# Optimization experiments

Measured on AMD Instinct MI355X. Metric: run time of the kernel, lower is better.

Reference implementation:

```python
import jax, jax.numpy as jnp
import numpy as np

T, B, I, H = 100, 64, 256, 512


def setup_inputs() -> dict:
    key = jax.random.key(0)
    ks = jax.random.split(key, 7)
    # torch kaiming_uniform_(a=sqrt(5)) + fan_in bias init -> uniform(-1/sqrt(fan_in), 1/sqrt(fan_in))
    b_ih = 1.0 / np.sqrt(I)
    b_hh = 1.0 / np.sqrt(H)
    return {
        "input": jax.random.normal(ks[0], (T, B, I), jnp.float32),
        "initial_h": jax.random.normal(ks[1], (B, H), jnp.float32),
        "initial_c": jax.random.normal(ks[2], (B, H), jnp.float32),
        "weight_ih": jax.random.uniform(ks[3], (4 * H, I), jnp.float32, -b_ih, b_ih),
        "weight_hh": jax.random.uniform(ks[4], (4 * H, H), jnp.float32, -b_hh, b_hh),
        "bias_ih": jax.random.uniform(ks[5], (4 * H,), jnp.float32, -b_ih, b_ih),
        "bias_hh": jax.random.uniform(ks[6], (4 * H,), jnp.float32, -b_hh, b_hh),
    }


def reference(input, initial_h, initial_c, weight_ih, weight_hh, bias_ih, bias_hh):
    Bsz, Isz = input.shape[1], input.shape[2]
    Hs = initial_h.shape[1]

    def step(carry, x_t):
        hx, cx, ev_ih, ev_hh, ev_b = carry
        # standard LSTM gates, torch gate order: i, f, g, o
        gates = x_t @ weight_ih.T + hx @ weight_hh.T + bias_ih + bias_hh  # [B,4H]
        i_g, f_g, g_g, o_g = jnp.split(gates, 4, axis=1)
        i = jax.nn.sigmoid(i_g)
        f = jax.nn.sigmoid(f_g)
        g = jnp.tanh(g_g)
        o = jax.nn.sigmoid(o_g)
        cy = f * cx + i * g
        hy = o * jnp.tanh(cy)
        # e-prop instantaneous derivatives of c_t wrt the i/f/g pre-activations
        d_i = g * i * (1.0 - i)          # [B,H]
        d_f = cx * f * (1.0 - f)
        d_g = i * (1.0 - g * g)
        d = jnp.concatenate([d_i, d_f, d_g], axis=1)[:, :, None]  # [B,3H,1]
        f3 = jnp.tile(f, (1, 3))[:, :, None]                      # [B,3H,1]
        # eligibility-trace recursion: ev_t = f_t * ev_{t-1} + d_t (outer) input
        ev_ih = f3 * ev_ih + d * x_t[:, None, :]   # [B,3H,I]
        ev_hh = f3 * ev_hh + d * hx[:, None, :]    # [B,3H,H]
        ev_b = f3 * ev_b + d                       # [B,3H,1]
        return (hy, cy, ev_ih, ev_hh, ev_b), hy

    ev_ih0 = jnp.zeros((Bsz, 3 * Hs, Isz), input.dtype)
    ev_hh0 = jnp.zeros((Bsz, 3 * Hs, Hs), input.dtype)
    ev_b0 = jnp.zeros((Bsz, 3 * Hs, 1), input.dtype)
    (hx, cx, ev_ih, ev_hh, ev_b), outputs = jax.lax.scan(
        step, (initial_h, initial_c, ev_ih0, ev_hh0, ev_b0), input
    )
    return outputs, cx, ev_ih, ev_hh, ev_b
```

## Files before the change

kernel.cpp:

```cpp
#include <hip/hip_runtime.h>
#include <math.h>

#define TT 100
#define BB 64
#define II 256
#define HH 512
#define G4H 2048
#define G3H 1536

#define OFF_GT    0
#define OFF_HBUF  13107200
#define OFF_FBUF  16416768
#define OFF_DBUF  19693568
#define OFF_CT    29523968
#define OFF_XT    29556736
#define OFF_WIHT  31195136
#define OFF_WHHT  31719424

#define O_OUT   0
#define O_CX    3276800
#define O_EVIH  3309568
#define O_EVHH  28475392
#define O_EVB   78807040

__global__ __launch_bounds__(256) void tp64(const float* __restrict__ src,
                                            float* __restrict__ dst,
                                            int R, int C,
                                            long sstride, long dstride) {
  __shared__ float tile[64][65];
  src += (long)blockIdx.z * sstride;
  dst += (long)blockIdx.z * dstride;
  int r0 = blockIdx.y * 64, c0 = blockIdx.x * 64;
  int tx = threadIdx.x & 15, tq = threadIdx.x >> 4;
#pragma unroll
  for (int p = 0; p < 4; ++p) {
    int rl = p * 16 + tq;
    float4 v = *(const float4*)(src + (long)(r0 + rl) * C + c0 + tx * 4);
    tile[rl][tx * 4 + 0] = v.x; tile[rl][tx * 4 + 1] = v.y;
    tile[rl][tx * 4 + 2] = v.z; tile[rl][tx * 4 + 3] = v.w;
  }
  __syncthreads();
#pragma unroll
  for (int p = 0; p < 4; ++p) {
    int cl = p * 16 + tq;
    float4 v;
    v.x = tile[tx * 4 + 0][cl]; v.y = tile[tx * 4 + 1][cl];
    v.z = tile[tx * 4 + 2][cl]; v.w = tile[tx * 4 + 3][cl];
    *(float4*)(dst + (long)(c0 + cl) * R + r0 + tx * 4) = v;
  }
}

__global__ __launch_bounds__(256) void make_whhg(const float* __restrict__ WhhT,
                                                 float* __restrict__ WhhG) {
  int gid = blockIdx.x * 256 + threadIdx.x;
  int k = gid >> 11, j = gid & 2047;
  float v = WhhT[gid];
  WhhG[(long)k * G4H + ((j & 511) << 2) + (j >> 9)] = v;
}

template <int BK, int KTILES, bool BIAS, bool ZSHIFT>
__global__ __launch_bounds__(256) void gemm_tn(
    const float* __restrict__ A, long batchA, int lda,
    const float* __restrict__ Z, long batchZ, int ldz,
    const float* __restrict__ Z0, long batchZ0,
    float* __restrict__ C, long batchC, int ldc,
    const float* __restrict__ bia, const float* __restrict__ bib) {
  __shared__ float As[BK][64];
  __shared__ float Zs[BK][64];
  int tid = threadIdx.x;
  int tn = tid & 15, tm = tid >> 4;
  int m0 = blockIdx.x * 64, n0 = blockIdx.y * 64;
  long bz = blockIdx.z;
  const float* Ab = A + bz * batchA + m0;
  const float* Zb = Z + bz * batchZ + n0;
  const float* Z0b = ZSHIFT ? (Z0 + bz * batchZ0 + n0) : nullptr;
  float acc[4][4] = {};
  for (int kt = 0; kt < KTILES; ++kt) {
    int k0 = kt * BK;
#pragma unroll
    for (int p = tid; p < BK * 64; p += 256) {
      int r = p >> 6, c = p & 63;
      int k = k0 + r;
      As[r][c] = Ab[(long)k * lda + c];
      const float* zr;
      if (ZSHIFT)
        zr = (k == 0) ? Z0b : (Zb + (long)(k - 1) * ldz);
      else
        zr = Zb + (long)k * ldz;
      Zs[r][c] = zr[c];
    }
    __syncthreads();
#pragma unroll 4
    for (int kk = 0; kk < BK; ++kk) {
      float4 a = *(const float4*)&As[kk][tm * 4];
      float4 z = *(const float4*)&Zs[kk][tn * 4];
      float av[4] = {a.x, a.y, a.z, a.w};
      float zv[4] = {z.x, z.y, z.z, z.w};
#pragma unroll
      for (int q = 0; q < 4; ++q)
#pragma unroll
        for (int r = 0; r < 4; ++r)
          acc[q][r] = fmaf(av[q], zv[r], acc[q][r]);
    }
    __syncthreads();
  }
  float* Cb = C + bz * batchC + n0 + tn * 4;
#pragma unroll
  for (int q = 0; q < 4; ++q) {
    int m = m0 + tm * 4 + q;
    float bv = BIAS ? (bia[m] + bib[m]) : 0.f;
    float4 v;
    v.x = acc[q][0] + bv; v.y = acc[q][1] + bv;
    v.z = acc[q][2] + bv; v.w = acc[q][3] + bv;
    *(float4*)(Cb + (long)m * ldc) = v;
  }
}

__global__ __launch_bounds__(512) void lstm_step2(const float* __restrict__ G_T,
                                                  const float* __restrict__ WhhG,
                                                  float* __restrict__ Hbuf,
                                                  float* __restrict__ cT,
                                                  float* __restrict__ Fbuf,
                                                  float* __restrict__ Dbuf,
                                                  int t) {
  __shared__ float red[2][4][4][64];
  int tid = threadIdx.x;
  int lane = tid & 63;
  int wave = __builtin_amdgcn_readfirstlane(tid >> 6);
  int hl = wave & 1, kp = wave >> 1;
  int hh = blockIdx.x * 2 + hl;
  float a0 = 0.f, a1 = 0.f, a2 = 0.f, a3 = 0.f;
  const float* hp = Hbuf + (long)t * (HH * BB) + kp * 128 * BB + lane;
  const float* wp = WhhG + (long)(kp * 128) * G4H + hh * 4;
#pragma unroll 4
  for (int k = 0; k < 128; ++k) {
    float h = hp[(long)k * BB];
    float4 w = *(const float4*)(wp + (long)k * G4H);
    a0 = fmaf(w.x, h, a0);
    a1 = fmaf(w.y, h, a1);
    a2 = fmaf(w.z, h, a2);
    a3 = fmaf(w.w, h, a3);
  }
  red[hl][kp][0][lane] = a0;
  red[hl][kp][1][lane] = a1;
  red[hl][kp][2][lane] = a2;
  red[hl][kp][3][lane] = a3;
  __syncthreads();
  if (tid < 128) {
    int b = tid & 63, h2 = tid >> 6;
    int hhx = blockIdx.x * 2 + h2;
    const float* gp = G_T + (long)t * (G4H * BB) + hhx * BB + b;
    float g[4];
#pragma unroll
    for (int q = 0; q < 4; ++q)
      g[q] = gp[(long)q * (HH * BB)] + red[h2][0][q][b] + red[h2][1][q][b] +
             red[h2][2][q][b] + red[h2][3][q][b];
    float ig = 1.f / (1.f + expf(-g[0]));
    float fg = 1.f / (1.f + expf(-g[1]));
    float gg = tanhf(g[2]);
    float og = 1.f / (1.f + expf(-g[3]));
    int idx = hhx * BB + b;
    float co = cT[idx];
    float cy = fg * co + ig * gg;
    cT[idx] = cy;
    Hbuf[(long)(t + 1) * (HH * BB) + idx] = og * tanhf(cy);
    Fbuf[(long)t * (HH * BB) + idx] = fg;
    float* dp = Dbuf + (long)t * (G3H * BB) + idx;
    dp[0] = gg * ig * (1.f - ig);
    dp[HH * BB] = co * fg * (1.f - fg);
    dp[2 * HH * BB] = ig * (1.f - gg * gg);
  }
}

__global__ __launch_bounds__(256) void suffix_scale(float* __restrict__ Dbuf,
                                                    const float* __restrict__ Fbuf,
                                                    float* __restrict__ evb) {
  int g = blockIdx.x * 256 + threadIdx.x;
  int b = g & 63, hh = g >> 6;
  float P = 1.f, e0 = 0.f, e1 = 0.f, e2 = 0.f;
#pragma unroll 2
  for (int t = TT - 1; t >= 0; --t) {
    float* dp = Dbuf + (long)t * (G3H * BB) + hh * BB + b;
    float v0 = dp[0] * P, v1 = dp[HH * BB] * P, v2 = dp[2 * HH * BB] * P;
    dp[0] = v0; dp[HH * BB] = v1; dp[2 * HH * BB] = v2;
    e0 += v0; e1 += v1; e2 += v2;
    P *= Fbuf[(long)t * (HH * BB) + hh * BB + b];
  }
  evb[b * G3H + hh] = e0;
  evb[b * G3H + HH + hh] = e1;
  evb[b * G3H + 2 * HH + hh] = e2;
}

extern "C" void kernel_launch(void* const* d_in, const int* in_sizes, int n_in,
                              void* d_out, int out_size, void* d_ws, size_t ws_size,
                              hipStream_t stream) {
  const float* x   = (const float*)d_in[0];
  const float* h0  = (const float*)d_in[1];
  const float* c0  = (const float*)d_in[2];
  const float* Wih = (const float*)d_in[3];
  const float* Whh = (const float*)d_in[4];
  const float* bih = (const float*)d_in[5];
  const float* bhh = (const float*)d_in[6];
  float* out = (float*)d_out;
  float* ws = (float*)d_ws;

  float* G_T   = ws + OFF_GT;
  float* DbufT = ws + OFF_GT;
  float* Hbuf  = ws + OFF_HBUF;
  float* Fbuf  = ws + OFF_FBUF;
  float* Dbuf  = ws + OFF_DBUF;
  float* cT    = ws + OFF_CT;
  float* xT    = ws + OFF_XT;
  float* WhhG  = ws + OFF_XT;
  float* WihT  = ws + OFF_WIHT;
  float* WhhT  = ws + OFF_WHHT;

  tp64<<<dim3(II / 64, G4H / 64, 1), 256, 0, stream>>>(Wih, WihT, G4H, II, 0, 0);
  tp64<<<dim3(HH / 64, G4H / 64, 1), 256, 0, stream>>>(Whh, WhhT, G4H, HH, 0, 0);
  tp64<<<dim3(II / 64, 1, TT), 256, 0, stream>>>(x, xT, BB, II, BB * II, BB * II);
  tp64<<<dim3(HH / 64, 1, 1), 256, 0, stream>>>(h0, Hbuf, BB, HH, 0, 0);
  tp64<<<dim3(HH / 64, 1, 1), 256, 0, stream>>>(c0, cT, BB, HH, 0, 0);

  gemm_tn<64, 4, true, false><<<dim3(G4H / 64, 1, TT), 256, 0, stream>>>(
      WihT, 0, G4H, xT, (long)II * BB, BB, nullptr, 0,
      G_T, (long)G4H * BB, BB, bih, bhh);

  make_whhg<<<dim3(HH * G4H / 256, 1, 1), 256, 0, stream>>>(WhhT, WhhG);

  for (int t = 0; t < TT; ++t) {
    lstm_step2<<<dim3(HH / 2, 1, 1), 512, 0, stream>>>(G_T, WhhG, Hbuf, cT,
                                                       Fbuf, Dbuf, t);
  }

  suffix_scale<<<dim3(HH * BB / 256, 1, 1), 256, 0, stream>>>(Dbuf, Fbuf,
                                                              out + O_EVB);

  tp64<<<dim3(1, TT * G3H / 64, 1), 256, 0, stream>>>(Dbuf, DbufT, TT * G3H, BB,
                                                      0, 0);

  tp64<<<dim3(1, HH / 64, TT), 256, 0, stream>>>(Hbuf + HH * BB, out + O_OUT,
                                                 HH, BB, HH * BB, HH * BB);
  tp64<<<dim3(1, HH / 64, 1), 256, 0, stream>>>(cT, out + O_CX, HH, BB, 0, 0);

  gemm_tn<20, 5, false, false><<<dim3(G3H / 64, II / 64, BB), 256, 0, stream>>>(
      DbufT, (long)TT * G3H, G3H, x, (long)II, (long)BB * II, nullptr, 0,
      out + O_EVIH, (long)G3H * II, II, nullptr, nullptr);

  gemm_tn<20, 5, false, true><<<dim3(G3H / 64, HH / 64, BB), 256, 0, stream>>>(
      DbufT, (long)TT * G3H, G3H, out + O_OUT, (long)HH, (long)BB * HH,
      h0, (long)HH,
      out + O_EVHH, (long)G3H * HH, HH, nullptr, nullptr);
}
```

Baseline: 1.768 ms.

## Replace per-timestep LSTM launches with persistent cooperative kernel and grid barrier

Runs the recurrent loop as one persistent cooperative kernel of 256 blocks that synchronise between timesteps with a global atomic barrier, instead of launching 100 kernels. Each block keeps its 8 rows of W_hh resident in LDS and the cell state in registers, so weight reloads, the transpose and reorder kernels, and launch overhead go away. In exchange it relies on all 256 blocks being co-resident, and the spin barrier adds per-step latency.

```diff
diff --git a/kernel.cpp b/kernel.cpp
--- a/kernel.cpp
+++ b/kernel.cpp
@@ -15,7 +15,7 @@
 #define OFF_CT    29523968
 #define OFF_XT    29556736
 #define OFF_WIHT  31195136
-#define OFF_WHHT  31719424
+#define OFF_BAR   31719424
 
 #define O_OUT   0
 #define O_CX    3276800
@@ -48,14 +48,6 @@
     v.z = tile[tx * 4 + 2][cl]; v.w = tile[tx * 4 + 3][cl];
     *(float4*)(dst + (long)(c0 + cl) * R + r0 + tx * 4) = v;
   }
-}
-
-__global__ __launch_bounds__(256) void make_whhg(const float* __restrict__ WhhT,
-                                                 float* __restrict__ WhhG) {
-  int gid = blockIdx.x * 256 + threadIdx.x;
-  int k = gid >> 11, j = gid & 2047;
-  float v = WhhT[gid];
-  WhhG[(long)k * G4H + ((j & 511) << 2) + (j >> 9)] = v;
 }
 
 template <int BK, int KTILES, bool BIAS, bool ZSHIFT>
@@ -116,59 +108,114 @@
   }
 }
 
-__global__ __launch_bounds__(512) void lstm_step2(const float* __restrict__ G_T,
-                                                  const float* __restrict__ WhhG,
-                                                  float* __restrict__ Hbuf,
-                                                  float* __restrict__ cT,
-                                                  float* __restrict__ Fbuf,
-                                                  float* __restrict__ Dbuf,
-                                                  int t) {
-  __shared__ float red[2][4][4][64];
+__global__ void zero_bar(int* bar) {
+  if (threadIdx.x < 2) bar[threadIdx.x] = 0;
+}
+
+__device__ __forceinline__ void grid_barrier(int* bar, int nblk) {
+  __syncthreads();
+  if (threadIdx.x == 0) {
+    __threadfence();
+    int gen = __hip_atomic_load(bar + 1, __ATOMIC_RELAXED,
+                                __HIP_MEMORY_SCOPE_AGENT);
+    int arr = __hip_atomic_fetch_add(bar, 1, __ATOMIC_ACQ_REL,
+                                     __HIP_MEMORY_SCOPE_AGENT);
+    if (arr == nblk - 1) {
+      __hip_atomic_store(bar, 0, __ATOMIC_RELAXED, __HIP_MEMORY_SCOPE_AGENT);
+      __hip_atomic_store(bar + 1, gen + 1, __ATOMIC_RELEASE,
+                         __HIP_MEMORY_SCOPE_AGENT);
+    } else {
+      while (__hip_atomic_load(bar + 1, __ATOMIC_ACQUIRE,
+                               __HIP_MEMORY_SCOPE_AGENT) == gen) {
+        __builtin_amdgcn_s_sleep(1);
+      }
+    }
+  }
+  __syncthreads();
+}
+
+__global__ __launch_bounds__(512) void lstm_persist(
+    const float* __restrict__ G_T, const float* __restrict__ Whh,
+    float* __restrict__ Hbuf, const float* __restrict__ c0,
+    float* __restrict__ cT, float* __restrict__ Fbuf,
+    float* __restrict__ Dbuf, int* bar) {
+  __shared__ float Wlds[512][8];
+  __shared__ float red[8][8][64];
+  __shared__ float gl[8][64];
   int tid = threadIdx.x;
   int lane = tid & 63;
-  int wave = __builtin_amdgcn_readfirstlane(tid >> 6);
-  int hl = wave & 1, kp = wave >> 1;
-  int hh = blockIdx.x * 2 + hl;
-  float a0 = 0.f, a1 = 0.f, a2 = 0.f, a3 = 0.f;
-  const float* hp = Hbuf + (long)t * (HH * BB) + kp * 128 * BB + lane;
-  const float* wp = WhhG + (long)(kp * 128) * G4H + hh * 4;
-#pragma unroll 4
-  for (int k = 0; k < 128; ++k) {
-    float h = hp[(long)k * BB];
-    float4 w = *(const float4*)(wp + (long)k * G4H);
-    a0 = fmaf(w.x, h, a0);
-    a1 = fmaf(w.y, h, a1);
-    a2 = fmaf(w.z, h, a2);
-    a3 = fmaf(w.w, h, a3);
-  }
-  red[hl][kp][0][lane] = a0;
-  red[hl][kp][1][lane] = a1;
-  red[hl][kp][2][lane] = a2;
-  red[hl][kp][3][lane] = a3;
+  int w = __builtin_amdgcn_readfirstlane(tid >> 6);
+  int hh0 = blockIdx.x * 2;
+
+#pragma unroll
+  for (int row = 0; row < 8; ++row) {
+    int hl = row >> 2, g = row & 3;
+    Wlds[tid][row] = Whh[((g << 9) + hh0 + hl) * 512 + tid];
+  }
+
+  float creg = 0.f;
+  if (tid < 128) creg = c0[(tid & 63) * HH + hh0 + (tid >> 6)];
   __syncthreads();
+
+  for (int t = 0; t < TT; ++t) {
+    const float* hp = Hbuf + (long)t * (HH * BB) + (w * 64) * BB + lane;
+    const float* wl = &Wlds[w * 64][0];
+    float a0 = 0.f, a1 = 0.f, a2 = 0.f, a3 = 0.f;
+    float a4 = 0.f, a5 = 0.f, a6 = 0.f, a7 = 0.f;
+#pragma unroll 8
+    for (int k = 0; k < 64; ++k) {
+      float h = hp[k * BB];
+      float4 wa = *(const float4*)(wl + k * 8);
+      float4 wb = *(const float4*)(wl + k * 8 + 4);
+      a0 = fmaf(wa.x, h, a0);
+      a1 = fmaf(wa.y, h, a1);
+      a2 = fmaf(wa.z, h, a2);
+      a3 = fmaf(wa.w, h, a3);
+      a4 = fmaf(wb.x, h, a4);
+      a5 = fmaf(wb.y, h, a5);
+      a6 = fmaf(wb.z, h, a6);
+      a7 = fmaf(wb.w, h, a7);
+    }
+    red[w][0][lane] = a0; red[w][1][lane] = a1;
+    red[w][2][lane] = a2; red[w][3][lane] = a3;
+    red[w][4][lane] = a4; red[w][5][lane] = a5;
+    red[w][6][lane] = a6; red[w][7][lane] = a7;
+    __syncthreads();
+
+    {
+      int jj = w, b = lane;
+      int jg = ((jj & 3) << 9) + hh0 + (jj >> 2);
+      float s = G_T[(long)t * (G4H * BB) + (long)jg * BB + b];
+#pragma unroll
+      for (int ww = 0; ww < 8; ++ww) s += red[ww][jj][b];
+      gl[jj][b] = s;
+    }
+    __syncthreads();
+
+    if (tid < 128) {
+      int b = tid & 63, h2 = tid >> 6;
+      int hhx = hh0 + h2;
+      float ig = 1.f / (1.f + expf(-gl[h2 * 4 + 0][b]));
+      float fg = 1.f / (1.f + expf(-gl[h2 * 4 + 1][b]));
+      float gg = tanhf(gl[h2 * 4 + 2][b]);
+      float og = 1.f / (1.f + expf(-gl[h2 * 4 + 3][b]));
+      float co = creg;
+      float cy = fg * co + ig * gg;
+      creg = cy;
+      int idx = hhx * BB + b;
+      Hbuf[(long)(t + 1) * (HH * BB) + idx] = og * tanhf(cy);
+      Fbuf[(long)t * (HH * BB) + idx] = fg;
+      float* dp = Dbuf + (long)t * (G3H * BB) + idx;
+      dp[0] = gg * ig * (1.f - ig);
+      dp[HH * BB] = co * fg * (1.f - fg);
+      dp[2 * HH * BB] = ig * (1.f - gg * gg);
+    }
+    grid_barrier(bar, 256);
+  }
+
   if (tid < 128) {
     int b = tid & 63, h2 = tid >> 6;
-    int hhx = blockIdx.x * 2 + h2;
-    const float* gp = G_T + (long)t * (G4H * BB) + hhx * BB + b;
-    float g[4];
-#pragma unroll
-    for (int q = 0; q < 4; ++q)
-      g[q] = gp[(long)q * (HH * BB)] + red[h2][0][q][b] + red[h2][1][q][b] +
-             red[h2][2][q][b] + red[h2][3][q][b];
-    float ig = 1.f / (1.f + expf(-g[0]));
-    float fg = 1.f / (1.f + expf(-g[1]));
-    float gg = tanhf(g[2]);
-    float og = 1.f / (1.f + expf(-g[3]));
-    int idx = hhx * BB + b;
-    float co = cT[idx];
-    float cy = fg * co + ig * gg;
-    cT[idx] = cy;
-    Hbuf[(long)(t + 1) * (HH * BB) + idx] = og * tanhf(cy);
-    Fbuf[(long)t * (HH * BB) + idx] = fg;
-    float* dp = Dbuf + (long)t * (G3H * BB) + idx;
-    dp[0] = gg * ig * (1.f - ig);
-    dp[HH * BB] = co * fg * (1.f - fg);
-    dp[2 * HH * BB] = ig * (1.f - gg * gg);
+    cT[(hh0 + h2) * BB + b] = creg;
   }
 }
 
@@ -211,25 +258,25 @@
   float* Dbuf  = ws + OFF_DBUF;
   float* cT    = ws + OFF_CT;
   float* xT    = ws + OFF_XT;
-  float* WhhG  = ws + OFF_XT;
   float* WihT  = ws + OFF_WIHT;
-  float* WhhT  = ws + OFF_WHHT;
+  int*   bar   = (int*)(ws + OFF_BAR);
 
   tp64<<<dim3(II / 64, G4H / 64, 1), 256, 0, stream>>>(Wih, WihT, G4H, II, 0, 0);
-  tp64<<<dim3(HH / 64, G4H / 64, 1), 256, 0, stream>>>(Whh, WhhT, G4H, HH, 0, 0);
   tp64<<<dim3(II / 64, 1, TT), 256, 0, stream>>>(x, xT, BB, II, BB * II, BB * II);
   tp64<<<dim3(HH / 64, 1, 1), 256, 0, stream>>>(h0, Hbuf, BB, HH, 0, 0);
-  tp64<<<dim3(HH / 64, 1, 1), 256, 0, stream>>>(c0, cT, BB, HH, 0, 0);
 
   gemm_tn<64, 4, true, false><<<dim3(G4H / 64, 1, TT), 256, 0, stream>>>(
       WihT, 0, G4H, xT, (long)II * BB, BB, nullptr, 0,
       G_T, (long)G4H * BB, BB, bih, bhh);
 
-  make_whhg<<<dim3(HH * G4H / 256, 1, 1), 256, 0, stream>>>(WhhT, WhhG);
-
-  for (int t = 0; t < TT; ++t) {
-    lstm_step2<<<dim3(HH / 2, 1, 1), 512, 0, stream>>>(G_T, WhhG, Hbuf, cT,
-                                                       Fbuf, Dbuf, t);
+  zero_bar<<<1, 64, 0, stream>>>(bar);
+  {
+    const float* a0 = G_T; const float* a1 = Whh; float* a2 = Hbuf;
+    const float* a3 = c0; float* a4 = cT; float* a5 = Fbuf; float* a6 = Dbuf;
+    int* a7 = bar;
+    void* args[] = {&a0, &a1, &a2, &a3, &a4, &a5, &a6, &a7};
+    hipLaunchCooperativeKernel((void*)lstm_persist, dim3(256), dim3(512), args,
+                               0, stream);
   }
 
   suffix_scale<<<dim3(HH * BB / 256, 1, 1), 256, 0, stream>>>(Dbuf, Fbuf,
```

Result: slower. 3.519 ms (+99.0%).
